# Optimization experiments

Hardware: AMD Instinct MI355X
Metric: run time of the kernel (lower is better)

The kernel has to match this reference:

```python
import jax, jax.numpy as jnp
import numpy as np
from jax import lax

EPS = 1e-5
DN = ('NCHW', 'OIHW', 'NCHW')


def _bn(x, gamma, beta, mean, var):
    # eval-mode BatchNorm2d over channel dim (axis=1)
    s = gamma / jnp.sqrt(var + EPS)
    return x * s[None, :, None, None] + (beta - mean * s)[None, :, None, None]


def setup_inputs() -> dict:
    key = jax.random.key(0)
    ks = jax.random.split(key, 12)
    B, Cin, C, H, W, NC = 128, 2048, 512, 14, 14, 200
    return {
        'feature': jax.random.normal(ks[0], (B, Cin, H, W), jnp.float32),
        'w_reduce': jax.random.normal(ks[1], (C, Cin, 1, 1), jnp.float32) * 0.02,
        'b_reduce': jax.random.normal(ks[2], (C,), jnp.float32) * 0.02,
        'bn1_gamma': jnp.ones((C,), jnp.float32),
        'bn1_beta': jnp.zeros((C,), jnp.float32),
        'bn1_mean': jax.random.normal(ks[3], (C,), jnp.float32) * 0.02,
        'bn1_var': jax.random.uniform(ks[4], (C,), jnp.float32),
        'w3': jax.random.normal(ks[5], (C, C, 3, 3), jnp.float32) * 0.02,
        'b3': jax.random.normal(ks[6], (C,), jnp.float32) * 0.02,
        'bn2_gamma': jnp.ones((C,), jnp.float32),
        'bn2_beta': jnp.zeros((C,), jnp.float32),
        'bn2_mean': jax.random.normal(ks[7], (C,), jnp.float32) * 0.02,
        'bn2_var': jax.random.uniform(ks[8], (C,), jnp.float32),
        'fc1_w': jax.random.normal(ks[9], (NC, C), jnp.float32) * 0.02,
        'fc1_b': jnp.zeros((NC,), jnp.float32),
        'fc2_w': jax.random.normal(ks[10], (NC, NC), jnp.float32) * 0.02,
        'fc2_b': jnp.zeros((NC,), jnp.float32),
    }


def reference(feature, w_reduce, b_reduce, bn1_gamma, bn1_beta, bn1_mean, bn1_var,
              w3, b3, bn2_gamma, bn2_beta, bn2_mean, bn2_var,
              fc1_w, fc1_b, fc2_w, fc2_b):
    B, _, H, W = feature.shape
    C = w_reduce.shape[0]  # 512
    # reduce: 1x1 conv + BN + ReLU
    f = lax.conv_general_dilated(feature, w_reduce, (1, 1), 'VALID', dimension_numbers=DN)
    f = f + b_reduce[None, :, None, None]
    f = jax.nn.relu(_bn(f, bn1_gamma, bn1_beta, bn1_mean, bn1_var))
    x = f.reshape(B, C, H * W)  # [B, 512, 196]
    # channel affinity + softmax(-xxt) over last dim (= the per-row loop)
    xxt = jnp.einsum('bcn,bdn->bcd', x, x)  # [B, 512, 512]
    a = jax.nn.softmax(-xxt, axis=2)
    y = jnp.einsum('bcd,bdn->bcn', a, x).reshape(B, C, H, W)
    # conv3: 3x3 conv + BN + ReLU + global avg pool
    z = lax.conv_general_dilated(y, w3, (1, 1), 'SAME', dimension_numbers=DN)
    z = z + b3[None, :, None, None]
    z = jax.nn.relu(_bn(z, bn2_gamma, bn2_beta, bn2_mean, bn2_var))
    z = jnp.mean(z, axis=(2, 3))  # [B, 512]
    # fc_channel: Linear -> ReLU -> Linear
    h = jax.nn.relu(z @ fc1_w.T + fc1_b)
    sf = h @ fc2_w.T + fc2_b
    return sf
```

## Files before the change

### kernel.cpp

```cpp
#include <hip/hip_runtime.h>

typedef __attribute__((ext_vector_type(8))) short bf16x8;
typedef __attribute__((ext_vector_type(4))) float f32x4;
typedef __attribute__((ext_vector_type(4))) short short4v;
typedef __attribute__((ext_vector_type(2))) short short2v;

__device__ __forceinline__ unsigned short f2bf(float x){
  unsigned u = __float_as_uint(x);
  return (unsigned short)((u + 0x7FFFu + ((u>>16)&1u)) >> 16);
}
__device__ __forceinline__ float bf2f(unsigned short b){
  return __uint_as_float(((unsigned)b)<<16);
}

typedef const __attribute__((address_space(1))) void* gas_t;
typedef __attribute__((address_space(3))) void* las_t;
__device__ __forceinline__ void gl16(const void* g, void* l){
  __builtin_amdgcn_global_load_lds((gas_t)g, (las_t)l, 16, 0, 0);
}

static constexpr size_t O_FHI  = 0;
static constexpr size_t O_FLO  = 102760448;
static constexpr size_t O_XHI  = 205520896;
static constexpr size_t O_XLO  = 239075328;
static constexpr size_t O_XT   = 272629760;
static constexpr size_t O_AMAT = 301989888;
static constexpr size_t O_WH   = 369098752;
static constexpr size_t O_WL   = 371195904;
static constexpr size_t O_W3B  = 373293056;
static constexpr size_t O_PAR  = 378011648;
static constexpr size_t O_FC1T = 378019840;
static constexpr size_t O_FC2T = 378429440;
static constexpr size_t O_ZBAR = 378589440;

__global__ __launch_bounds__(256) void k_prep(
    const float* wr, unsigned short* wh, unsigned short* wl,
    const float* w3, unsigned short* w3c,
    const float* fc1w, float* fc1T, const float* fc2w, float* fc2T,
    const float* br, const float* g1, const float* be1, const float* m1, const float* v1,
    const float* b3, const float* g2, const float* be2, const float* m2, const float* v2,
    float* par, unsigned short* xhi, unsigned short* xlo){
  int blk = blockIdx.x, t = threadIdx.x;
  if (blk < 4096){
    int idx = blk*256 + t;
    int c = idx >> 11, k = idx & 2047;
    float v = wr[(size_t)c*2048 + k];
    unsigned short h = f2bf(v);
    wh[(size_t)c*2048+k] = h; wl[(size_t)c*2048+k] = f2bf(v - bf2f(h));
  } else if (blk < 13312){
    int i = (blk-4096)*256 + t;
    int co = i / 4608, k = i - co*4608;
    int ci0b = k / 576, r2 = k - ci0b*576;
    int tap = r2 >> 6, cio = r2 & 63;
    w3c[(((size_t)ci0b*9+tap)*512+co)*64+cio] =
        f2bf(w3[((size_t)co*512 + ci0b*64+cio)*9 + tap]);
  } else if (blk < 13712){
    int i = (blk-13312)*256 + t;
    int k = i/200, j = i - k*200;
    fc1T[i] = fc1w[j*512+k];
  } else if (blk < 13869){
    int i = (blk-13712)*256 + t;
    if (i < 40000){ int k = i/200, j = i - k*200; fc2T[i] = fc2w[j*200+k]; }
  } else if (blk < 13871){
    int c = (blk-13869)*256 + t;
    if (c < 512){
      float s1 = g1[c]*rsqrtf(v1[c]+1e-5f);
      par[c] = s1; par[512+c] = (br[c]-m1[c])*s1 + be1[c];
      float s2 = g2[c]*rsqrtf(v2[c]+1e-5f);
      par[1024+c] = s2; par[1536+c] = (b3[c]-m2[c])*s2 + be2[c];
    }
  } else {
    int rr = (blk-13871)*256 + t;
    float4 z = {0.f,0.f,0.f,0.f};
    float4* a = (float4*)(xhi + (size_t)rr*256 + 192);
    float4* bq = (float4*)(xlo + (size_t)rr*256 + 192);
    #pragma unroll
    for (int q=0;q<8;++q){ a[q]=z; bq[q]=z; }
  }
}

__global__ __launch_bounds__(256) void k_featT(const float* __restrict__ feat,
        unsigned short* __restrict__ fhi, unsigned short* __restrict__ flo){
  __shared__ float tile[64][33];
  int b = blockIdx.z;
  int ci0 = blockIdx.y*64, p0 = blockIdx.x*32;
  int t = threadIdx.x;
  int j = t & 31, i0 = t >> 5;
  for (int rep=0; rep<8; ++rep){
    int i = rep*8 + i0;
    int p = p0 + j;
    tile[i][j] = (p<196) ? feat[((size_t)b*2048 + ci0 + i)*196 + p] : 0.f;
  }
  __syncthreads();
  int j2 = t & 31;
  int jj0 = t >> 5;
  for (int rep=0; rep<4; ++rep){
    int jj = rep*8 + jj0;
    int p = p0 + jj;
    if (p < 196){
      float v0 = tile[2*j2][jj], v1 = tile[2*j2+1][jj];
      unsigned short h0 = f2bf(v0), h1 = f2bf(v1);
      unsigned short l0 = f2bf(v0 - bf2f(h0)), l1 = f2bf(v1 - bf2f(h1));
      size_t o = ((size_t)b*196 + p)*2048 + ci0 + 2*j2;
      short2v hv; hv[0]=(short)h0; hv[1]=(short)h1;
      short2v lv; lv[0]=(short)l0; lv[1]=(short)l1;
      *(short2v*)(fhi + o) = hv;
      *(short2v*)(flo + o) = lv;
    }
  }
}

__global__ __launch_bounds__(256, 1) void k_conv1(
    const unsigned short* __restrict__ fhi, const unsigned short* __restrict__ flo,
    const unsigned short* __restrict__ wh,  const unsigned short* __restrict__ wl,
    const float* __restrict__ par,
    unsigned short* __restrict__ xhi, unsigned short* __restrict__ xlo,
    unsigned short* __restrict__ xT){
  __shared__ char lds[147456];
  int lin = blockIdx.x;
  int sz  = (lin&7)*49 + (lin>>3);
  int mt = sz&3;
  int gt = sz>>2;
  int c0 = mt*128;
  size_t g0 = (size_t)gt*256;
  int t = threadIdx.x, lane = t&63, wv = t>>6;
  int fq = (lane>>4)&3, fr = lane&15;
  f32x4 acc[8][4] = {};

  auto STAGE = [&](int it, char* buf){
    #pragma unroll
    for (int jj=0; jj<12; ++jj){
      const unsigned short* src; int ldsoff;
      if (jj < 4){
        int g = (jj&1)*256 + t;
        int row = g>>2;
        int cs = ((g&3) ^ ((row>>1)&3))*8;
        src = ((jj<2)? wh : wl) + (size_t)(c0+row)*2048 + it*32 + cs;
        ldsoff = ((jj<2)? 0 : 8192) + g*16;
      } else {
        int g = (jj&3)*256 + t;
        int row = g>>2;
        int cs = ((g&3) ^ ((row>>1)&3))*8;
        src = ((jj<8)? fhi : flo) + (g0+row)*2048 + it*32 + cs;
        ldsoff = ((jj<8)? 16384 : 32768) + g*16;
      }
      gl16(src, buf + ldsoff);
    }
  };

  char* b0 = lds;
  char* b1 = lds + 49152;
  char* b2 = lds + 98304;
  STAGE(0, b0);
  STAGE(1, b1);

  for (int it=0; it<64; ++it){
    if (it < 63) { asm volatile("s_waitcnt vmcnt(12)" ::: "memory"); }
    else         { asm volatile("s_waitcnt vmcnt(0)"  ::: "memory"); }
    __builtin_amdgcn_s_barrier();
    __builtin_amdgcn_sched_barrier(0);
    if (it+2 < 64) STAGE(it+2, b2);
    {
      const char* A = b0; const char* B = b0 + 16384;
      bf16x8 ah[8], al[8];
      #pragma unroll
      for (int m=0;m<8;++m){
        int row = m*16 + fr;
        int off = row*64 + ((fq*16) ^ (((row>>1)&3)<<4));
        ah[m] = *(const bf16x8*)(A + off);
        al[m] = *(const bf16x8*)(A + 8192 + off);
      }
      __builtin_amdgcn_s_setprio(1);
      #pragma unroll
      for (int n=0;n<4;++n){
        int row = wv*64 + n*16 + fr;
        int off = row*64 + ((fq*16) ^ (((row>>1)&3)<<4));
        bf16x8 bh = *(const bf16x8*)(B + off);
        bf16x8 bl = *(const bf16x8*)(B + 16384 + off);
        #pragma unroll
        for (int m=0;m<8;++m){
          acc[m][n] = __builtin_amdgcn_mfma_f32_16x16x32_bf16(ah[m], bh, acc[m][n],0,0,0);
          acc[m][n] = __builtin_amdgcn_mfma_f32_16x16x32_bf16(ah[m], bl, acc[m][n],0,0,0);
          acc[m][n] = __builtin_amdgcn_mfma_f32_16x16x32_bf16(al[m], bh, acc[m][n],0,0,0);
        }
      }
      __builtin_amdgcn_s_setprio(0);
    }
    char* tmp = b0; b0 = b1; b1 = b2; b2 = tmp;
  }

  const float* s1 = par; const float* t1 = par+512;
  for (int m=0;m<8;++m){
    int cb = c0 + m*16 + fq*4;
    float sc[4], sh[4];
    for (int j=0;j<4;++j){ sc[j]=s1[cb+j]; sh[j]=t1[cb+j]; }
    for (int n=0;n<4;++n){
      int gg = (int)g0 + wv*64 + n*16 + fr;
      int b = gg/196, p = gg - b*196;
      unsigned short hs[4];
      for (int j=0;j<4;++j){
        float v = fmaxf(acc[m][n][j]*sc[j]+sh[j], 0.f);
        unsigned short h = f2bf(v);
        hs[j] = h;
        size_t ic = (size_t)b*512 + cb + j;
        xhi[ic*256 + p] = h;
        xlo[ic*256 + p] = f2bf(v - bf2f(h));
      }
      *(short4v*)(xT + ((size_t)b*224 + p)*512 + cb) = *(short4v*)hs;
    }
  }
}

__global__ __launch_bounds__(256) void k_xxt(const unsigned short* __restrict__ xhi,
        const unsigned short* __restrict__ xlo, float* __restrict__ xxt){
  __shared__ char lds[32768];
  char* Als = lds; char* Bls = lds + 16384;
  int lin = blockIdx.x;
  int sz  = (lin&7)*160 + (lin>>3);
  int b = sz/10, sub = sz - b*10;
  unsigned mtp = (3u<<18)|(2u<<16)|(2u<<14)|(1u<<12)|(1u<<10)|(1u<<8)|(0u<<6)|(0u<<4)|(0u<<2)|0u;
  unsigned ntp = (3u<<18)|(3u<<16)|(2u<<14)|(3u<<12)|(2u<<10)|(1u<<8)|(3u<<6)|(2u<<4)|(1u<<2)|0u;
  int mt = (mtp>>(2*sub))&3, nt = (ntp>>(2*sub))&3;
  int c0 = mt*128, d0 = nt*128;
  int t = threadIdx.x, lane = t&63, wid = t>>6, wm = wid&1, wn = wid>>1;
  int fq = lane>>4, fr = lane&15;
  f32x4 acc[4][4] = {};
  for (int it=0; it<12; ++it){
    int seg = it>>2, kk0 = (it&3)*64;
    const unsigned short* As = (seg<2) ? xhi : xlo;
    const unsigned short* Bs = (seg==1) ? xlo : xhi;
    __syncthreads();
    #pragma unroll
    for (int r=0;r<4;++r){
      int L = r*256 + t;
      int row = L>>3, cs = ((L&7)^(row&7))*8;
      gl16(As + ((size_t)b*512 + c0 + row)*256 + kk0 + cs, Als + L*16);
      gl16(Bs + ((size_t)b*512 + d0 + row)*256 + kk0 + cs, Bls + L*16);
    }
    __syncthreads();
    #pragma unroll
    for (int ks=0; ks<2; ++ks){
      int kb = ks*64 + fq*16;
      bf16x8 af[4];
      #pragma unroll
      for (int m=0;m<4;++m){
        int row = wm*64 + m*16 + fr;
        af[m] = *(const bf16x8*)(Als + row*128 + (kb ^ ((row&7)<<4)));
      }
      #pragma unroll
      for (int n=0;n<4;++n){
        int row = wn*64 + n*16 + fr;
        bf16x8 bff = *(const bf16x8*)(Bls + row*128 + (kb ^ ((row&7)<<4)));
        #pragma unroll
        for (int m=0;m<4;++m)
          acc[m][n] = __builtin_amdgcn_mfma_f32_16x16x32_bf16(af[m], bff, acc[m][n],0,0,0);
      }
    }
  }
  for (int m=0;m<4;++m){
    int cb = c0 + wm*64 + m*16 + fq*4;
    for (int n=0;n<4;++n){
      int d = d0 + wn*64 + n*16 + fr;
      *(float4*)(xxt + ((size_t)b*512 + d)*512 + cb) = *(float4*)&acc[m][n];
    }
  }
  if (mt != nt){
    for (int m=0;m<4;++m){
      int cb = c0 + wm*64 + m*16 + fq*4;
      for (int n=0;n<4;++n){
        int d = d0 + wn*64 + n*16 + fr;
        for (int jj=0;jj<4;++jj)
          xxt[((size_t)b*512 + cb + jj)*512 + d] = acc[m][n][jj];
      }
    }
  }
}

__global__ __launch_bounds__(256) void k_softmax(const float* __restrict__ xxt, unsigned short* __restrict__ amat){
  int row = blockIdx.x*4 + (threadIdx.x>>6);
  int lane = threadIdx.x & 63;
  const float* src = xxt + (size_t)row*512 + lane*8;
  float4 v0 = *(const float4*)src;
  float4 v1 = *(const float4*)(src+4);
  float mn = fminf(fminf(fminf(v0.x,v0.y),fminf(v0.z,v0.w)),
                   fminf(fminf(v1.x,v1.y),fminf(v1.z,v1.w)));
  for (int m=32; m; m>>=1) mn = fminf(mn, __shfl_xor(mn, m, 64));
  float e[8];
  e[0]=__expf(mn-v0.x); e[1]=__expf(mn-v0.y); e[2]=__expf(mn-v0.z); e[3]=__expf(mn-v0.w);
  e[4]=__expf(mn-v1.x); e[5]=__expf(mn-v1.y); e[6]=__expf(mn-v1.z); e[7]=__expf(mn-v1.w);
  float s = e[0]+e[1]+e[2]+e[3]+e[4]+e[5]+e[6]+e[7];
  for (int m=32; m; m>>=1) s += __shfl_xor(s, m, 64);
  float inv = 1.f/s;
  short4v p0, p1;
  for (int q=0;q<4;++q) p0[q] = (short)f2bf(e[q]*inv);
  for (int q=0;q<4;++q) p1[q] = (short)f2bf(e[4+q]*inv);
  unsigned short* dst = amat + (size_t)row*512 + lane*8;
  *(short4v*)dst = p0;
  *(short4v*)(dst+4) = p1;
}

__global__ __launch_bounds__(256) void k_pv(const unsigned short* __restrict__ amat,
        const unsigned short* __restrict__ xT, unsigned short* __restrict__ ypad){
  __shared__ char lds[30720];
  char* Als = lds; char* Bls = lds + 16384;
  int lin = blockIdx.x, per = gridDim.x>>3;
  int sz  = (lin&7)*per + (lin>>3);
  int b = sz>>3, sub = sz&7, mt = sub>>1, nt = sub&1;
  int c0 = mt*128, n0 = nt*112;
  int t = threadIdx.x, lane = t&63, wid = t>>6;
  int fq = lane>>4, fr = lane&15;
  {
    int r = t;
    int hi = r>>4, lo2 = r&15;
    if (hi==0||hi==15||lo2==0||lo2==15){
      float4 z = {0.f,0.f,0.f,0.f};
      float4* pz = (float4*)(ypad + (((size_t)b*8 + sub)*256 + r)*64);
      #pragma unroll
      for (int q=0;q<8;++q) pz[q] = z;
    }
  }
  f32x4 acc[2][7] = {};
  for (int it=0; it<8; ++it){
    int k0 = it*64;
    __syncthreads();
    #pragma unroll
    for (int r=0;r<4;++r){
      int L = r*256 + t;
      int row = L>>3, cs = ((L&7)^(row&7))*8;
      gl16(amat + ((size_t)b*512 + c0 + row)*512 + k0 + cs, Als + L*16);
    }
    #pragma unroll
    for (int r=0;r<4;++r){
      int L = r*256 + t;
      if (L < 896){
        int row = L>>3, cs = ((L&7)^(row&7))*8;
        gl16(xT + ((size_t)b*224 + n0 + row)*512 + k0 + cs, Bls + L*16);
      }
    }
    __syncthreads();
    #pragma unroll
    for (int ks=0; ks<2; ++ks){
      int kb = ks*64 + fq*16;
      bf16x8 af[2];
      #pragma unroll
      for (int m=0;m<2;++m){
        int row = wid*32 + m*16 + fr;
        af[m] = *(const bf16x8*)(Als + row*128 + (kb ^ ((row&7)<<4)));
      }
      #pragma unroll
      for (int n=0;n<7;++n){
        int row = n*16 + fr;
        bf16x8 bff = *(const bf16x8*)(Bls + row*128 + (kb ^ ((row&7)<<4)));
        #pragma unroll
        for (int m=0;m<2;++m)
          acc[m][n] = __builtin_amdgcn_mfma_f32_16x16x32_bf16(af[m], bff, acc[m][n],0,0,0);
      }
    }
  }
  for (int m=0;m<2;++m){
    int cb = c0 + wid*32 + m*16 + fq*4;
    int ci0b = cb>>6, cio = cb&63;
    for (int n=0;n<7;++n){
      int p = n0 + n*16 + fr;
      if (p < 196){
        int hh = p/14, wwp = p - hh*14;
        int prow = (hh+1)*16 + (wwp+1);
        short4v pk;
        for (int j=0;j<4;++j) pk[j] = (short)f2bf(acc[m][n][j]);
        *(short4v*)(ypad + (((size_t)b*8 + ci0b)*256 + prow)*64 + cio) = pk;
      }
    }
  }
}

__global__ __launch_bounds__(512, 4) void k_conv3(const unsigned short* __restrict__ ypad,
        const unsigned short* __restrict__ w3c, const float* __restrict__ par,
        float* __restrict__ zbar){
  __shared__ char lds[65536];
  char* WIN = lds;
  char* AB0 = lds + 32768;
  char* AB1 = lds + 49152;
  int bx = blockIdx.x;
  int xcd = bx&7, jj2 = bx>>3;
  int b = xcd*16 + (jj2>>2), cot = jj2&3;
  int c0 = cot*128;
  int t = threadIdx.x, lane = t&63, w = t>>6;
  int wm = w>>1, wn = w&1;
  int fq = lane>>4, fr = lane&15;
  int frB = (fr<14) ? fr : 13;
  bool pok = (fr<14);
  f32x4 acc[2][7] = {};
  for (int ci0=0; ci0<8; ++ci0){
    const unsigned short* wsrc = ypad + ((size_t)(b*8 + ci0)*256)*64;
    #pragma unroll
    for (int r=0;r<4;++r){
      int L = r*512 + t;
      int row = L>>3, cs = ((L&7)^(row&7))*8;
      gl16(wsrc + row*64 + cs, WIN + L*16);
    }
    {
      const unsigned short* asrc = w3c + ((size_t)(ci0*9 + 0)*512 + c0)*64;
      #pragma unroll
      for (int r=0;r<2;++r){
        int L = r*512 + t;
        int row = L>>3, cs = ((L&7)^(row&7))*8;
        gl16(asrc + row*64 + cs, AB0 + L*16);
      }
    }
    __syncthreads();
    for (int tap=0; tap<9; ++tap){
      char* Acur = (tap&1) ? AB1 : AB0;
      char* Anxt = (tap&1) ? AB0 : AB1;
      if (tap < 8){
        const unsigned short* asrc = w3c + ((size_t)(ci0*9 + tap+1)*512 + c0)*64;
        #pragma unroll
        for (int r=0;r<2;++r){
          int L = r*512 + t;
          int row = L>>3, cs = ((L&7)^(row&7))*8;
          gl16(asrc + row*64 + cs, Anxt + L*16);
        }
      }
      int kh = tap/3, kw = tap - kh*3;
      bf16x8 ah[2][2];
      #pragma unroll
      for (int ks=0;ks<2;++ks)
        #pragma unroll
        for (int m=0;m<2;++m){
          int row = wm*32 + m*16 + fr;
          ah[ks][m] = *(const bf16x8*)(Acur + row*128 + (((ks*4+fq)^(row&7))<<4));
        }
      int col = frB + kw;
      __builtin_amdgcn_s_setprio(1);
      #pragma unroll
      for (int n=0;n<7;++n){
        int prow = (wn*7 + n + kh)*16 + col;
        #pragma unroll
        for (int ks=0;ks<2;++ks){
          bf16x8 bf = *(const bf16x8*)(WIN + prow*128 + (((ks*4+fq)^(prow&7))<<4));
          acc[0][n] = __builtin_amdgcn_mfma_f32_16x16x32_bf16(ah[ks][0], bf, acc[0][n],0,0,0);
          acc[1][n] = __builtin_amdgcn_mfma_f32_16x16x32_bf16(ah[ks][1], bf, acc[1][n],0,0,0);
        }
      }
      __builtin_amdgcn_s_setprio(0);
      __syncthreads();
    }
  }
  const float* s2 = par+1024; const float* t2 = par+1536;
  float ps[2][4];
  #pragma unroll
  for (int m=0;m<2;++m){
    int cb = c0 + wm*32 + m*16 + fq*4;
    #pragma unroll
    for (int j=0;j<4;++j){
      float sc = s2[cb+j], sh = t2[cb+j];
      float s = 0.f;
      #pragma unroll
      for (int n=0;n<7;++n)
        s += fmaxf(acc[m][n][j]*sc + sh, 0.f);
      ps[m][j] = pok ? s : 0.f;
    }
  }
  #pragma unroll
  for (int off=1; off<16; off<<=1)
    #pragma unroll
    for (int m=0;m<2;++m)
      #pragma unroll
      for (int j=0;j<4;++j)
        ps[m][j] += __shfl_xor(ps[m][j], off, 64);
  float* part = (float*)lds;
  if (fr == 0){
    #pragma unroll
    for (int m=0;m<2;++m)
      #pragma unroll
      for (int j=0;j<4;++j)
        part[wn*128 + wm*32 + m*16 + fq*4 + j] = ps[m][j];
  }
  __syncthreads();
  if (t < 128)
    zbar[(size_t)b*512 + c0 + t] = part[t] + part[128 + t];
}

__global__ __launch_bounds__(256) void k_fc(const float* __restrict__ zbar,
        const float* __restrict__ fc1T, const float* __restrict__ fc1b,
        const float* __restrict__ fc2T, const float* __restrict__ fc2b,
        float* __restrict__ out){
  __shared__ float zb[512];
  __shared__ float hl[200];
  int b = blockIdx.x, t = threadIdx.x;
  zb[t]     = zbar[(size_t)b*512 + t]       * (1.f/196.f);
  zb[t+256] = zbar[(size_t)b*512 + t + 256] * (1.f/196.f);
  __syncthreads();
  if (t < 200){
    float acc = fc1b[t];
    for (int k=0;k<512;++k) acc += zb[k]*fc1T[k*200+t];
    hl[t] = fmaxf(acc, 0.f);
  }
  __syncthreads();
  if (t < 200){
    float acc = fc2b[t];
    for (int k=0;k<200;++k) acc += hl[k]*fc2T[k*200+t];
    out[(size_t)b*200 + t] = acc;
  }
}

extern "C" void kernel_launch(void* const* d_in, const int* in_sizes, int n_in,
                              void* d_out, int out_size, void* d_ws, size_t ws_size,
                              hipStream_t stream) {
  const float* feature  = (const float*)d_in[0];
  const float* w_reduce = (const float*)d_in[1];
  const float* b_reduce = (const float*)d_in[2];
  const float* g1  = (const float*)d_in[3];
  const float* be1 = (const float*)d_in[4];
  const float* m1  = (const float*)d_in[5];
  const float* v1  = (const float*)d_in[6];
  const float* w3  = (const float*)d_in[7];
  const float* b3  = (const float*)d_in[8];
  const float* g2  = (const float*)d_in[9];
  const float* be2 = (const float*)d_in[10];
  const float* m2  = (const float*)d_in[11];
  const float* v2  = (const float*)d_in[12];
  const float* fc1w = (const float*)d_in[13];
  const float* fc1b = (const float*)d_in[14];
  const float* fc2w = (const float*)d_in[15];
  const float* fc2b = (const float*)d_in[16];

  char* ws = (char*)d_ws;
  unsigned short* fhi  = (unsigned short*)(ws + O_FHI);
  unsigned short* flo  = (unsigned short*)(ws + O_FLO);
  float*          xxt  = (float*)(ws + O_FHI);
  unsigned short* xhi  = (unsigned short*)(ws + O_XHI);
  unsigned short* xlo  = (unsigned short*)(ws + O_XLO);
  unsigned short* ypad = (unsigned short*)(ws + O_XLO);
  unsigned short* xT   = (unsigned short*)(ws + O_XT);
  unsigned short* amat = (unsigned short*)(ws + O_AMAT);
  unsigned short* wh   = (unsigned short*)(ws + O_WH);
  unsigned short* wl   = (unsigned short*)(ws + O_WL);
  unsigned short* w3c  = (unsigned short*)(ws + O_W3B);
  float* par  = (float*)(ws + O_PAR);
  float* fc1T = (float*)(ws + O_FC1T);
  float* fc2T = (float*)(ws + O_FC2T);
  float* zbar = (float*)(ws + O_ZBAR);

  k_prep<<<14127, 256, 0, stream>>>(w_reduce, wh, wl, w3, w3c,
      fc1w, fc1T, fc2w, fc2T,
      b_reduce, g1, be1, m1, v1, b3, g2, be2, m2, v2, par, xhi, xlo);

  k_featT<<<dim3(7,32,128), 256, 0, stream>>>(feature, fhi, flo);
  k_conv1<<<392, 256, 0, stream>>>(fhi, flo, wh, wl, par, xhi, xlo, xT);

  k_xxt<<<1280, 256, 0, stream>>>(xhi, xlo, xxt);
  k_softmax<<<16384, 256, 0, stream>>>(xxt, amat);

  k_pv<<<1024, 256, 0, stream>>>(amat, xT, ypad);
  k_conv3<<<512, 512, 0, stream>>>(ypad, w3c, par, zbar);
  k_fc<<<128, 256, 0, stream>>>(zbar, fc1T, fc1b, fc2T, fc2b, (float*)d_out);
}
```

Before: 660.4 us.

## Shrink conv1 tile to 128x128 with two waves and double buffering

The 1x1 reduce-conv GEMM now uses blocks of 128 threads that each compute a 128-channel by 128-pixel tile, launched as 784 blocks instead of 392. The three-stage LDS ring (144KB) is replaced by a two-buffer scheme (64KB), with a full vmcnt(0) wait and barrier at the end of each iteration. The smaller LDS footprint should let more than one block share a CU, giving better occupancy and load balance across CUs. In exchange, prefetch depth drops, each wave does less reuse of the staged A tile, and the per-iteration full wait may expose global-load latency.

```diff
diff --git a/kernel.cpp b/kernel.cpp
--- a/kernel.cpp
+++ b/kernel.cpp
@@ -110,83 +110,76 @@
   }
 }
 
-__global__ __launch_bounds__(256, 1) void k_conv1(
+__global__ __launch_bounds__(128, 1) void k_conv1(
     const unsigned short* __restrict__ fhi, const unsigned short* __restrict__ flo,
     const unsigned short* __restrict__ wh,  const unsigned short* __restrict__ wl,
     const float* __restrict__ par,
     unsigned short* __restrict__ xhi, unsigned short* __restrict__ xlo,
     unsigned short* __restrict__ xT){
-  __shared__ char lds[147456];
+  __shared__ char lds[65536];
+  char* BUF0 = lds;
+  char* BUF1 = lds + 32768;
   int lin = blockIdx.x;
-  int sz  = (lin&7)*49 + (lin>>3);
+  int sz  = (lin&7)*98 + (lin>>3);
   int mt = sz&3;
   int gt = sz>>2;
   int c0 = mt*128;
-  size_t g0 = (size_t)gt*256;
+  size_t g0 = (size_t)gt*128;
   int t = threadIdx.x, lane = t&63, wv = t>>6;
   int fq = (lane>>4)&3, fr = lane&15;
   f32x4 acc[8][4] = {};
 
   auto STAGE = [&](int it, char* buf){
     #pragma unroll
-    for (int jj=0; jj<12; ++jj){
-      const unsigned short* src; int ldsoff;
-      if (jj < 4){
-        int g = (jj&1)*256 + t;
-        int row = g>>2;
-        int cs = ((g&3) ^ ((row>>1)&3))*8;
-        src = ((jj<2)? wh : wl) + (size_t)(c0+row)*2048 + it*32 + cs;
-        ldsoff = ((jj<2)? 0 : 8192) + g*16;
-      } else {
-        int g = (jj&3)*256 + t;
-        int row = g>>2;
-        int cs = ((g&3) ^ ((row>>1)&3))*8;
-        src = ((jj<8)? fhi : flo) + (g0+row)*2048 + it*32 + cs;
-        ldsoff = ((jj<8)? 16384 : 32768) + g*16;
-      }
-      gl16(src, buf + ldsoff);
+    for (int jj=0; jj<16; ++jj){
+      int arr = jj>>2;
+      int g = (jj&3)*128 + t;
+      int row = g>>2;
+      int cs = ((g&3) ^ ((row>>1)&3))*8;
+      const unsigned short* src;
+      if (arr==0)      src = wh  + (size_t)(c0+row)*2048 + it*32 + cs;
+      else if (arr==1) src = wl  + (size_t)(c0+row)*2048 + it*32 + cs;
+      else if (arr==2) src = fhi + (g0+row)*2048 + it*32 + cs;
+      else             src = flo + (g0+row)*2048 + it*32 + cs;
+      gl16(src, buf + arr*8192 + g*16);
     }
   };
 
-  char* b0 = lds;
-  char* b1 = lds + 49152;
-  char* b2 = lds + 98304;
-  STAGE(0, b0);
-  STAGE(1, b1);
+  STAGE(0, BUF0);
+  asm volatile("s_waitcnt vmcnt(0)" ::: "memory");
+  __builtin_amdgcn_s_barrier();
+  __builtin_amdgcn_sched_barrier(0);
 
   for (int it=0; it<64; ++it){
-    if (it < 63) { asm volatile("s_waitcnt vmcnt(12)" ::: "memory"); }
-    else         { asm volatile("s_waitcnt vmcnt(0)"  ::: "memory"); }
+    char* cur = (it&1) ? BUF1 : BUF0;
+    char* nxt = (it&1) ? BUF0 : BUF1;
+    if (it < 63) STAGE(it+1, nxt);
+    bf16x8 ah[8], al[8];
+    #pragma unroll
+    for (int m=0;m<8;++m){
+      int row = m*16 + fr;
+      int off = row*64 + ((fq*16) ^ (((row>>1)&3)<<4));
+      ah[m] = *(const bf16x8*)(cur + off);
+      al[m] = *(const bf16x8*)(cur + 8192 + off);
+    }
+    __builtin_amdgcn_s_setprio(1);
+    #pragma unroll
+    for (int n=0;n<4;++n){
+      int row = wv*64 + n*16 + fr;
+      int off = row*64 + ((fq*16) ^ (((row>>1)&3)<<4));
+      bf16x8 bh = *(const bf16x8*)(cur + 16384 + off);
+      bf16x8 bl = *(const bf16x8*)(cur + 24576 + off);
+      #pragma unroll
+      for (int m=0;m<8;++m){
+        acc[m][n] = __builtin_amdgcn_mfma_f32_16x16x32_bf16(ah[m], bh, acc[m][n],0,0,0);
+        acc[m][n] = __builtin_amdgcn_mfma_f32_16x16x32_bf16(ah[m], bl, acc[m][n],0,0,0);
+        acc[m][n] = __builtin_amdgcn_mfma_f32_16x16x32_bf16(al[m], bh, acc[m][n],0,0,0);
+      }
+    }
+    __builtin_amdgcn_s_setprio(0);
+    asm volatile("s_waitcnt vmcnt(0)" ::: "memory");
     __builtin_amdgcn_s_barrier();
     __builtin_amdgcn_sched_barrier(0);
-    if (it+2 < 64) STAGE(it+2, b2);
-    {
-      const char* A = b0; const char* B = b0 + 16384;
-      bf16x8 ah[8], al[8];
-      #pragma unroll
-      for (int m=0;m<8;++m){
-        int row = m*16 + fr;
-        int off = row*64 + ((fq*16) ^ (((row>>1)&3)<<4));
-        ah[m] = *(const bf16x8*)(A + off);
-        al[m] = *(const bf16x8*)(A + 8192 + off);
-      }
-      __builtin_amdgcn_s_setprio(1);
-      #pragma unroll
-      for (int n=0;n<4;++n){
-        int row = wv*64 + n*16 + fr;
-        int off = row*64 + ((fq*16) ^ (((row>>1)&3)<<4));
-        bf16x8 bh = *(const bf16x8*)(B + off);
-        bf16x8 bl = *(const bf16x8*)(B + 16384 + off);
-        #pragma unroll
-        for (int m=0;m<8;++m){
-          acc[m][n] = __builtin_amdgcn_mfma_f32_16x16x32_bf16(ah[m], bh, acc[m][n],0,0,0);
-          acc[m][n] = __builtin_amdgcn_mfma_f32_16x16x32_bf16(ah[m], bl, acc[m][n],0,0,0);
-          acc[m][n] = __builtin_amdgcn_mfma_f32_16x16x32_bf16(al[m], bh, acc[m][n],0,0,0);
-        }
-      }
-      __builtin_amdgcn_s_setprio(0);
-    }
-    char* tmp = b0; b0 = b1; b1 = b2; b2 = tmp;
   }
 
   const float* s1 = par; const float* t1 = par+512;
@@ -546,7 +539,7 @@
       b_reduce, g1, be1, m1, v1, b3, g2, be2, m2, v2, par, xhi, xlo);
 
   k_featT<<<dim3(7,32,128), 256, 0, stream>>>(feature, fhi, flo);
-  k_conv1<<<392, 256, 0, stream>>>(fhi, flo, wh, wl, par, xhi, xlo, xT);
+  k_conv1<<<784, 128, 0, stream>>>(fhi, flo, wh, wl, par, xhi, xlo, xT);
 
   k_xxt<<<1280, 256, 0, stream>>>(xhi, xlo, xxt);
   k_softmax<<<16384, 256, 0, stream>>>(xxt, amat);
```

After: 654.7 us. Within noise of the previous version (-0.9%).
